# Optimization experiments

Measured on AMD Instinct MI355X. Metric: run time of the kernel, lower is better.

Reference implementation:

```python
import jax, jax.numpy as jnp
import numpy as np

EPS = 1e-5

def _layernorm(x, g, b):
    # LayerNorm over last dim (head_dim), eps=1e-5 like nn.LayerNorm
    mu = jnp.mean(x, axis=-1, keepdims=True)
    var = jnp.mean(jnp.square(x - mu), axis=-1, keepdims=True)
    return (x - mu) * jax.lax.rsqrt(var + EPS) * g + b

def _rotate_half(x):
    d = x.shape[-1] // 2
    return jnp.concatenate([-x[..., d:], x[..., :d]], axis=-1)

def _apply_rotary(x, cos, sin):
    # x: [B,S,H,D]; cos/sin: [S,D] broadcast over batch and heads
    c = cos[None, :, None, :]
    s = sin[None, :, None, :]
    return x * c + _rotate_half(x) * s

def setup_inputs() -> dict:
    key = jax.random.key(0)
    ks = jax.random.split(key, 16)
    B, S, Dm = 2, 1024, 2048
    H, Hkv, Dh = 16, 4, 128
    f = lambda k, shp: (jax.random.normal(k, shp, dtype=jnp.float32) * 0.02)
    return {
        "hidden_states": jax.random.normal(ks[0], (B, S, Dm), dtype=jnp.float32),
        "cos": jax.random.uniform(ks[1], (S, Dh), dtype=jnp.float32),
        "sin": jax.random.uniform(ks[2], (S, Dh), dtype=jnp.float32),
        "Wq": f(ks[3], (H * Dh, Dm)),   "bq": jnp.zeros((H * Dh,), jnp.float32),
        "Wk": f(ks[4], (Hkv * Dh, Dm)), "bk": jnp.zeros((Hkv * Dh,), jnp.float32),
        "Wv": f(ks[5], (Hkv * Dh, Dm)), "bv": jnp.zeros((Hkv * Dh,), jnp.float32),
        "Wo": f(ks[6], (Dm, H * Dh)),   "bo": jnp.zeros((Dm,), jnp.float32),
        "qn_g": jnp.ones((Dh,), jnp.float32), "qn_b": jnp.zeros((Dh,), jnp.float32),
        "kn_g": jnp.ones((Dh,), jnp.float32), "kn_b": jnp.zeros((Dh,), jnp.float32),
        "cu_seqlens": jnp.array([0, S, 2 * S], dtype=jnp.int32),
        "max_s": 1024,
    }

def reference(hidden_states, cos, sin, Wq, bq, Wk, bk, Wv, bv, Wo, bo,
              qn_g, qn_b, kn_g, kn_b, cu_seqlens, max_s):
    B, S, Dm = hidden_states.shape
    Dh = qn_g.shape[0]
    H = Wq.shape[0] // Dh
    Hkv = Wk.shape[0] // Dh
    scale = 1.0 / jnp.sqrt(jnp.float32(Dh))

    q = (hidden_states @ Wq.T + bq).reshape(B, S, H, Dh)
    k = (hidden_states @ Wk.T + bk).reshape(B, S, Hkv, Dh)
    v = (hidden_states @ Wv.T + bv).reshape(B, S, Hkv, Dh)

    q = _apply_rotary(_layernorm(q, qn_g, qn_b), cos, sin)
    k = _apply_rotary(_layernorm(k, kn_g, kn_b), cos, sin)

    # GQA: repeat_interleave kv heads to match q heads
    n_rep = H // Hkv
    if n_rep > 1:
        k = jnp.repeat(k, n_rep, axis=2)
        v = jnp.repeat(v, n_rep, axis=2)

    # scores: [B,H,S,S]
    scores = jnp.einsum('bqhd,bkhd->bhqk', q, k) * scale
    causal = jnp.tril(jnp.ones((S, S), dtype=bool))
    scores = jnp.where(causal[None, None], scores, jnp.finfo(scores.dtype).min)
    weights = jax.nn.softmax(scores, axis=-1)
    out = jnp.einsum('bhqk,bkhd->bqhd', weights, v).reshape(B, S, H * Dh)
    return out @ Wo.T + bo
```

## Files before the change

kernel.cpp:

```cpp
#include <hip/hip_runtime.h>
#include <cmath>

typedef __attribute__((ext_vector_type(8))) short bf16x8;
typedef __attribute__((ext_vector_type(4))) short s16x4;
typedef __attribute__((ext_vector_type(4))) float f32x4;

#define MFMA_BF16 __builtin_amdgcn_mfma_f32_16x16x32_bf16

__device__ __forceinline__ float bf2f(short s) {
    unsigned u = ((unsigned)(unsigned short)s) << 16;
    return __builtin_bit_cast(float, u);
}
__device__ __forceinline__ short f2bf(float f) {
    unsigned u = __builtin_bit_cast(unsigned, f);
    u += 0x7fffu + ((u >> 16) & 1u);
    return (short)(u >> 16);
}

__device__ __forceinline__ void gl_lds16(const short* gp, short* lp) {
    __builtin_amdgcn_global_load_lds(
        (const __attribute__((address_space(1))) unsigned int*)gp,
        (__attribute__((address_space(3))) unsigned int*)lp, 16, 0, 0);
}

__global__ __launch_bounds__(256) void cvt5(
    const float* s0, short* d0, int n0,
    const float* s1, short* d1, int n1,
    const float* s2, short* d2, int n2,
    const float* s3, short* d3, int n3,
    const float* s4, short* d4, int n4)
{
    long long i = (long long)blockIdx.x * 1024 + threadIdx.x * 4;
    const float* s; short* d;
    if      (i < n0)                  { s = s0; d = d0; }
    else if ((i -= n0) < n1)          { s = s1; d = d1; }
    else if ((i -= n1) < n2)          { s = s2; d = d2; }
    else if ((i -= n2) < n3)          { s = s3; d = d3; }
    else      { i -= n3;                s = s4; d = d4; }
    float4 v = *(const float4*)(s + i);
    s16x4 o;
    o[0] = f2bf(v.x); o[1] = f2bf(v.y); o[2] = f2bf(v.z); o[3] = f2bf(v.w);
    *(s16x4*)(d + i) = o;
}

__device__ __forceinline__ void stage128x32(
    const short* __restrict__ g, int gstride, short* l,
    int w, int lane, int kofs)
{
    const int row0 = 32 * w + (lane >> 2);
    const int kq   = (lane & 3) * 8;
#pragma unroll
    for (int i = 0; i < 2; i++) {
        const short* gp = g + (size_t)(row0 + 16 * i) * gstride + kofs + kq;
        short* lp = l + (32 * w + 16 * i) * 32 + lane * 8;
        gl_lds16(gp, lp);
    }
}

template <int MODE>
__global__ __launch_bounds__(256) void gemm128(
    const short* __restrict__ A, const short* __restrict__ W,
    const float* __restrict__ bq, const float* __restrict__ bk,
    const float* __restrict__ bv,
    short* __restrict__ qo, short* __restrict__ ko, short* __restrict__ vo,
    float* __restrict__ fo,
    int M, int K, int S, int Hkv, int Nq, int Nkv, int N)
{
    __shared__ __align__(16) short As[2][128 * 32];
    __shared__ __align__(16) short Bs[2][128 * 32];

    const int w    = threadIdx.x >> 6;
    const int lane = threadIdx.x & 63;
    const int l15  = lane & 15;
    const int quad = lane >> 4;
    const int wy   = w >> 1;
    const int wx   = w & 1;
    const int m0   = blockIdx.y * 128;
    const int n0   = blockIdx.x * 128;

    f32x4 acc[4][4];
#pragma unroll
    for (int i = 0; i < 4; i++)
#pragma unroll
        for (int j = 0; j < 4; j++) acc[i][j] = f32x4{0.f, 0.f, 0.f, 0.f};

    const short* Ab = A + (size_t)m0 * K;
    const short* Wb = W + (size_t)n0 * K;

    const int nk = K / 32;
    stage128x32(Ab, K, As[0], w, lane, 0);
    stage128x32(Wb, K, Bs[0], w, lane, 0);
    __syncthreads();

    for (int kt = 0; kt < nk; kt++) {
        const int cur = kt & 1;
        if (kt + 1 < nk) {
            stage128x32(Ab, K, As[cur ^ 1], w, lane, (kt + 1) * 32);
            stage128x32(Wb, K, Bs[cur ^ 1], w, lane, (kt + 1) * 32);
        }
        bf16x8 af[4], bfr[4];
#pragma unroll
        for (int i = 0; i < 4; i++)
            af[i] = *(const bf16x8*)(As[cur] + (wy * 64 + i * 16 + l15) * 32 + quad * 8);
#pragma unroll
        for (int j = 0; j < 4; j++)
            bfr[j] = *(const bf16x8*)(Bs[cur] + (wx * 64 + j * 16 + l15) * 32 + quad * 8);
#pragma unroll
        for (int i = 0; i < 4; i++)
#pragma unroll
            for (int j = 0; j < 4; j++)
                acc[i][j] = MFMA_BF16(af[i], bfr[j], acc[i][j], 0, 0, 0);
        __syncthreads();
    }

#pragma unroll
    for (int i = 0; i < 4; i++) {
#pragma unroll
        for (int j = 0; j < 4; j++) {
            const int col = n0 + wx * 64 + j * 16 + l15;
#pragma unroll
            for (int r = 0; r < 4; r++) {
                const int row = m0 + wy * 64 + i * 16 + quad * 4 + r;
                float v = acc[i][j][r];
                if constexpr (MODE == 0) {
                    if (col < Nq) {
                        qo[(size_t)row * Nq + col] = f2bf(v + bq[col]);
                    } else if (col < Nq + Nkv) {
                        int cn = col - Nq;
                        ko[(size_t)row * Nkv + cn] = f2bf(v + bk[cn]);
                    } else {
                        int cn = col - Nq - Nkv;
                        int b  = row / S, s = row - b * S;
                        int hk = cn >> 7, dh = cn & 127;
                        vo[(size_t)((b * Hkv + hk) * 128 + dh) * S + s] = f2bf(v + bv[cn]);
                    }
                } else {
                    fo[(size_t)row * N + col] = v + bq[col];
                }
            }
        }
    }
}

__global__ __launch_bounds__(256) void ln_rope(
    const short* __restrict__ X, short* __restrict__ Y,
    const float* __restrict__ g, const float* __restrict__ bta,
    const float* __restrict__ cosp, const float* __restrict__ sinp,
    int H, int S)
{
    const int gw   = blockIdx.x * 4 + (threadIdx.x >> 6);
    const int lane = threadIdx.x & 63;
    const int h  = gw % H;
    const int rs = gw / H;
    const int b  = rs / S;
    const int s  = rs - b * S;

    const short* x = X + ((size_t)rs * H + h) * 128;
    float x0 = bf2f(x[lane]), x1 = bf2f(x[lane + 64]);

    float sum = x0 + x1;
    float sq  = x0 * x0 + x1 * x1;
#pragma unroll
    for (int off = 32; off > 0; off >>= 1) {
        sum += __shfl_xor(sum, off, 64);
        sq  += __shfl_xor(sq, off, 64);
    }
    float mu  = sum * (1.f / 128.f);
    float var = sq * (1.f / 128.f) - mu * mu;
    float rinv = rsqrtf(var + 1e-5f);

    float y0 = (x0 - mu) * rinv * g[lane]      + bta[lane];
    float y1 = (x1 - mu) * rinv * g[lane + 64] + bta[lane + 64];

    float c0 = cosp[(size_t)s * 128 + lane];
    float c1 = cosp[(size_t)s * 128 + lane + 64];
    float s0 = sinp[(size_t)s * 128 + lane];
    float s1 = sinp[(size_t)s * 128 + lane + 64];

    float o0 = y0 * c0 - y1 * s0;
    float o1 = y1 * c1 + y0 * s1;

    short* yp = Y + ((size_t)(b * H + h) * S + s) * 128;
    yp[lane]      = f2bf(o0);
    yp[lane + 64] = f2bf(o1);
}

__global__ __launch_bounds__(256, 2) void attn(
    const short* __restrict__ Q, const short* __restrict__ Kt,
    const short* __restrict__ Vt, short* __restrict__ O,
    int S, int H, int Hkv, int nrep, float scale)
{
    __shared__ __align__(16) short Ks[2][16 * 512];
    __shared__ __align__(16) short Vs[2][16 * 512];
    __shared__ __align__(16) short P[4][16][72];

    const int w    = threadIdx.x >> 6;
    const int lane = threadIdx.x & 63;
    const int l15  = lane & 15;
    const int quad = lane >> 4;
    const int bh   = blockIdx.x;
    const int h    = bh % H;
    const int b    = bh / H;
    const int nyt  = gridDim.y;
    const int y    = blockIdx.y;
    const int qblk = (y < (nyt >> 1)) ? (nyt - 1 - y) : (y - (nyt >> 1));
    const int hk   = h / nrep;
    const int m0   = qblk * 64 + w * 16;
    const int qpos = m0 + l15;

    const short* qb = Q  + (size_t)(b * H + h) * S * 128;
    const short* kb = Kt + (size_t)(b * Hkv + hk) * S * 128;
    const short* vb = Vt + (size_t)(b * Hkv + hk) * 128 * S;

    auto stage = [&](int buf, int j0) {
#pragma unroll
        for (int i = 0; i < 8; i++) {
            if (w < 2) {
                const int s = w * 8 + i;
                const int t = s >> 2, c = s & 3;
                gl_lds16(kb + (size_t)(j0 + t * 16 + l15) * 128 + c * 32 + quad * 8,
                         Ks[buf] + s * 512 + lane * 8);
            } else {
                const int u = (w - 2) * 8 + i;
                const int c = u >> 1, hf = u & 1;
                gl_lds16(vb + (size_t)(c * 16 + l15) * S + j0 + hf * 32 + quad * 8,
                         Vs[buf] + u * 512 + lane * 8);
            }
        }
    };

    bf16x8 qf[4];
#pragma unroll
    for (int c = 0; c < 4; c++)
        qf[c] = *(const bf16x8*)(qb + (size_t)(m0 + l15) * 128 + c * 32 + quad * 8);

    f32x4 of[8];
#pragma unroll
    for (int c = 0; c < 8; c++) of[c] = f32x4{0.f, 0.f, 0.f, 0.f};
    float m_s = -1e30f, l_s = 0.f;
    const float c2 = scale * 1.44269504f;

    const int nkt = qblk + 1;
    stage(0, 0);
    __syncthreads();

    for (int kt = 0; kt < nkt; kt++) {
        const int cur = kt & 1;
        if (kt + 1 < nkt) stage(cur ^ 1, (kt + 1) * 64);

        const short* Kb = Ks[cur];
        const short* Vb = Vs[cur];
        const int j0 = kt * 64;

        f32x4 sc[4];
#pragma unroll
        for (int t = 0; t < 4; t++) sc[t] = f32x4{0.f, 0.f, 0.f, 0.f};
#pragma unroll
        for (int c = 0; c < 4; c++)
#pragma unroll
            for (int t = 0; t < 4; t++) {
                bf16x8 kf = *(const bf16x8*)(Kb + (t * 4 + c) * 512 + lane * 8);
                sc[t] = MFMA_BF16(kf, qf[c], sc[t], 0, 0, 0);
            }

        float v[4][4];
        float mx = -1e30f;
#pragma unroll
        for (int t = 0; t < 4; t++)
#pragma unroll
            for (int r = 0; r < 4; r++) {
                float s_ = sc[t][r];
                if (j0 + t * 16 + quad * 4 + r > qpos) s_ = -1e30f;
                v[t][r] = s_;
                mx = fmaxf(mx, s_);
            }
        mx = fmaxf(mx, __shfl_xor(mx, 16, 64));
        mx = fmaxf(mx, __shfl_xor(mx, 32, 64));
        float mnew  = fmaxf(m_s, mx);
        float mc    = mnew * c2;
        float alpha = exp2f(m_s * c2 - mc);
        float sum = 0.f;
        float p[4][4];
#pragma unroll
        for (int t = 0; t < 4; t++)
#pragma unroll
            for (int r = 0; r < 4; r++) {
                p[t][r] = exp2f(__builtin_fmaf(v[t][r], c2, -mc));
                sum += p[t][r];
            }
        sum += __shfl_xor(sum, 16, 64);
        sum += __shfl_xor(sum, 32, 64);
        l_s = l_s * alpha + sum;
        m_s = mnew;

#pragma unroll
        for (int c = 0; c < 8; c++) {
            f32x4 t = of[c];
            t[0] *= alpha; t[1] *= alpha; t[2] *= alpha; t[3] *= alpha;
            of[c] = t;
        }

#pragma unroll
        for (int t = 0; t < 4; t++) {
            s16x4 pk;
#pragma unroll
            for (int r = 0; r < 4; r++) pk[r] = f2bf(p[t][r]);
            *(s16x4*)(&P[w][l15][t * 16 + quad * 4]) = pk;
        }
        bf16x8 pb0 = *(const bf16x8*)(&P[w][l15][quad * 8]);
        bf16x8 pb1 = *(const bf16x8*)(&P[w][l15][32 + quad * 8]);

#pragma unroll
        for (int c = 0; c < 8; c++) {
            bf16x8 vf0 = *(const bf16x8*)(Vb + (c * 2 + 0) * 512 + lane * 8);
            bf16x8 vf1 = *(const bf16x8*)(Vb + (c * 2 + 1) * 512 + lane * 8);
            of[c] = MFMA_BF16(vf0, pb0, of[c], 0, 0, 0);
            of[c] = MFMA_BF16(vf1, pb1, of[c], 0, 0, 0);
        }
        __syncthreads();
    }

    const int HDh = H * 128;
    const float rinv = 1.0f / l_s;
    short* orow = O + ((size_t)b * S + qpos) * HDh + h * 128;
#pragma unroll
    for (int c = 0; c < 8; c++) {
        s16x4 ov;
#pragma unroll
        for (int r = 0; r < 4; r++) ov[r] = f2bf(of[c][r] * rinv);
        *(s16x4*)(orow + c * 16 + quad * 4) = ov;
    }
}

extern "C" void kernel_launch(void* const* d_in, const int* in_sizes, int n_in,
                              void* d_out, int out_size, void* d_ws, size_t ws_size,
                              hipStream_t stream) {
    const float* hs   = (const float*)d_in[0];
    const float* cosp = (const float*)d_in[1];
    const float* sinp = (const float*)d_in[2];
    const float* Wq   = (const float*)d_in[3];
    const float* bq   = (const float*)d_in[4];
    const float* Wk   = (const float*)d_in[5];
    const float* bk   = (const float*)d_in[6];
    const float* Wv   = (const float*)d_in[7];
    const float* bv   = (const float*)d_in[8];
    const float* Wo   = (const float*)d_in[9];
    const float* bo   = (const float*)d_in[10];
    const float* qg   = (const float*)d_in[11];
    const float* qb_  = (const float*)d_in[12];
    const float* kg   = (const float*)d_in[13];
    const float* kb_  = (const float*)d_in[14];

    const int Dh    = in_sizes[11];
    const int Dm    = in_sizes[10];
    const int HDh   = in_sizes[4];
    const int H     = HDh / Dh;
    const int HkvDh = in_sizes[6];
    const int Hkv   = HkvDh / Dh;
    const int S     = in_sizes[1] / Dh;
    const int B     = in_sizes[0] / (S * Dm);
    const int M     = B * S;
    const int nrep  = H / Hkv;

    char* ws = (char*)d_ws;
    short* hsb  = (short*)ws;  ws += (size_t)M * Dm      * 2;
    short* Wqb  = (short*)ws;  ws += (size_t)HDh * Dm    * 2;
    short* Wkb  = (short*)ws;  ws += (size_t)HkvDh * Dm  * 2;
    short* Wvb  = (short*)ws;  ws += (size_t)HkvDh * Dm  * 2;
    short* Wob  = (short*)ws;  ws += (size_t)Dm * HDh    * 2;
    short* qg16 = (short*)ws;  ws += (size_t)M * HDh     * 2;
    short* kg16 = (short*)ws;  ws += (size_t)M * HkvDh   * 2;
    short* qbuf = (short*)ws;  ws += (size_t)M * HDh     * 2;
    short* kbuf = (short*)ws;  ws += (size_t)M * HkvDh   * 2;
    short* vbuf = (short*)ws;  ws += (size_t)M * HkvDh   * 2;
    short* abuf = qg16;

    dim3 blk(256);
    const int n0 = M * Dm, n1 = HDh * Dm, n2 = HkvDh * Dm, n3 = HkvDh * Dm, n4 = Dm * HDh;
    cvt5<<<dim3((n0 + n1 + n2 + n3 + n4) / 1024), blk, 0, stream>>>(
        hs, hsb, n0, Wq, Wqb, n1, Wk, Wkb, n2, Wv, Wvb, n3, Wo, Wob, n4);

    const int Ntot = HDh + 2 * HkvDh;
    gemm128<0><<<dim3(Ntot / 128, M / 128), blk, 0, stream>>>(
        hsb, Wqb, bq, bk, bv, qg16, kg16, vbuf, nullptr,
        M, Dm, S, Hkv, HDh, HkvDh, Ntot);

    ln_rope<<<dim3(M * H / 4),   blk, 0, stream>>>(qg16, qbuf, qg, qb_, cosp, sinp, H,   S);
    ln_rope<<<dim3(M * Hkv / 4), blk, 0, stream>>>(kg16, kbuf, kg, kb_, cosp, sinp, Hkv, S);

    const float scale = 1.0f / sqrtf((float)Dh);
    attn<<<dim3(H * B, S / 64), blk, 0, stream>>>(qbuf, kbuf, vbuf, abuf, S, H, Hkv, nrep, scale);

    gemm128<1><<<dim3(Dm / 128, M / 128), blk, 0, stream>>>(
        abuf, Wob, bo, nullptr, nullptr, nullptr, nullptr, nullptr, (float*)d_out,
        M, HDh, S, Hkv, Dm, 0, Dm);
}
```

Baseline: 270.6 us.

## Shrink GEMM tile to 128x64 with XOR-swizzled LDS and fuse LN-rope launches

```diff
diff --git a/kernel.cpp b/kernel.cpp
--- a/kernel.cpp
+++ b/kernel.cpp
@@ -43,22 +43,8 @@
     *(s16x4*)(d + i) = o;
 }
 
-__device__ __forceinline__ void stage128x32(
-    const short* __restrict__ g, int gstride, short* l,
-    int w, int lane, int kofs)
-{
-    const int row0 = 32 * w + (lane >> 2);
-    const int kq   = (lane & 3) * 8;
-#pragma unroll
-    for (int i = 0; i < 2; i++) {
-        const short* gp = g + (size_t)(row0 + 16 * i) * gstride + kofs + kq;
-        short* lp = l + (32 * w + 16 * i) * 32 + lane * 8;
-        gl_lds16(gp, lp);
-    }
-}
-
 template <int MODE>
-__global__ __launch_bounds__(256) void gemm128(
+__global__ __launch_bounds__(256) void gemm_t(
     const short* __restrict__ A, const short* __restrict__ W,
     const float* __restrict__ bq, const float* __restrict__ bk,
     const float* __restrict__ bv,
@@ -66,8 +52,8 @@
     float* __restrict__ fo,
     int M, int K, int S, int Hkv, int Nq, int Nkv, int N)
 {
-    __shared__ __align__(16) short As[2][128 * 32];
-    __shared__ __align__(16) short Bs[2][128 * 32];
+    __shared__ __align__(16) short As[2][8 * 512];
+    __shared__ __align__(16) short Bs[2][4 * 512];
 
     const int w    = threadIdx.x >> 6;
     const int lane = threadIdx.x & 63;
@@ -76,39 +62,50 @@
     const int wy   = w >> 1;
     const int wx   = w & 1;
     const int m0   = blockIdx.y * 128;
-    const int n0   = blockIdx.x * 128;
-
-    f32x4 acc[4][4];
-#pragma unroll
-    for (int i = 0; i < 4; i++)
-#pragma unroll
-        for (int j = 0; j < 4; j++) acc[i][j] = f32x4{0.f, 0.f, 0.f, 0.f};
+    const int n0   = blockIdx.x * 64;
 
     const short* Ab = A + (size_t)m0 * K;
     const short* Wb = W + (size_t)n0 * K;
 
+    const int srow = lane >> 2;
+    const int scol = ((lane & 3) ^ (srow & 3)) * 8;
+    auto stage = [&](int buf, int kofs) {
+#pragma unroll
+        for (int i = 0; i < 2; i++) {
+            const int c = 2 * w + i;
+            gl_lds16(Ab + (size_t)(c * 16 + srow) * K + kofs + scol,
+                     As[buf] + c * 512 + lane * 8);
+        }
+        gl_lds16(Wb + (size_t)(w * 16 + srow) * K + kofs + scol,
+                 Bs[buf] + w * 512 + lane * 8);
+    };
+
+    f32x4 acc[4][2];
+#pragma unroll
+    for (int i = 0; i < 4; i++)
+#pragma unroll
+        for (int j = 0; j < 2; j++) acc[i][j] = f32x4{0.f, 0.f, 0.f, 0.f};
+
+    const int ridx = (l15 * 4 + (quad ^ (l15 & 3))) * 8;
     const int nk = K / 32;
-    stage128x32(Ab, K, As[0], w, lane, 0);
-    stage128x32(Wb, K, Bs[0], w, lane, 0);
+    stage(0, 0);
     __syncthreads();
 
     for (int kt = 0; kt < nk; kt++) {
         const int cur = kt & 1;
-        if (kt + 1 < nk) {
-            stage128x32(Ab, K, As[cur ^ 1], w, lane, (kt + 1) * 32);
-            stage128x32(Wb, K, Bs[cur ^ 1], w, lane, (kt + 1) * 32);
-        }
-        bf16x8 af[4], bfr[4];
+        if (kt + 1 < nk) stage(cur ^ 1, (kt + 1) * 32);
+
+        bf16x8 af[4], bfr[2];
 #pragma unroll
         for (int i = 0; i < 4; i++)
-            af[i] = *(const bf16x8*)(As[cur] + (wy * 64 + i * 16 + l15) * 32 + quad * 8);
-#pragma unroll
-        for (int j = 0; j < 4; j++)
-            bfr[j] = *(const bf16x8*)(Bs[cur] + (wx * 64 + j * 16 + l15) * 32 + quad * 8);
+            af[i] = *(const bf16x8*)(As[cur] + (wy * 4 + i) * 512 + ridx);
+#pragma unroll
+        for (int j = 0; j < 2; j++)
+            bfr[j] = *(const bf16x8*)(Bs[cur] + (wx * 2 + j) * 512 + ridx);
 #pragma unroll
         for (int i = 0; i < 4; i++)
 #pragma unroll
-            for (int j = 0; j < 4; j++)
+            for (int j = 0; j < 2; j++)
                 acc[i][j] = MFMA_BF16(af[i], bfr[j], acc[i][j], 0, 0, 0);
         __syncthreads();
     }
@@ -116,8 +113,8 @@
 #pragma unroll
     for (int i = 0; i < 4; i++) {
 #pragma unroll
-        for (int j = 0; j < 4; j++) {
-            const int col = n0 + wx * 64 + j * 16 + l15;
+        for (int j = 0; j < 2; j++) {
+            const int col = n0 + wx * 32 + j * 16 + l15;
 #pragma unroll
             for (int r = 0; r < 4; r++) {
                 const int row = m0 + wy * 64 + i * 16 + quad * 4 + r;
@@ -142,20 +139,26 @@
     }
 }
 
-__global__ __launch_bounds__(256) void ln_rope(
-    const short* __restrict__ X, short* __restrict__ Y,
-    const float* __restrict__ g, const float* __restrict__ bta,
+__global__ __launch_bounds__(256) void ln_rope2(
+    const short* __restrict__ Xq, short* __restrict__ Yq,
+    const short* __restrict__ Xk, short* __restrict__ Yk,
+    const float* __restrict__ qg, const float* __restrict__ qbe,
+    const float* __restrict__ kg, const float* __restrict__ kbe,
     const float* __restrict__ cosp, const float* __restrict__ sinp,
-    int H, int S)
+    int H, int Hkv, int S, int nq)
 {
-    const int gw   = blockIdx.x * 4 + (threadIdx.x >> 6);
+    int gw = blockIdx.x * 4 + (threadIdx.x >> 6);
     const int lane = threadIdx.x & 63;
-    const int h  = gw % H;
-    const int rs = gw / H;
+    const short* X; short* Y; const float* g; const float* bt; int Hc;
+    if (gw < nq) { X = Xq; Y = Yq; g = qg; bt = qbe; Hc = H; }
+    else { gw -= nq; X = Xk; Y = Yk; g = kg; bt = kbe; Hc = Hkv; }
+
+    const int h  = gw % Hc;
+    const int rs = gw / Hc;
     const int b  = rs / S;
     const int s  = rs - b * S;
 
-    const short* x = X + ((size_t)rs * H + h) * 128;
+    const short* x = X + ((size_t)rs * Hc + h) * 128;
     float x0 = bf2f(x[lane]), x1 = bf2f(x[lane + 64]);
 
     float sum = x0 + x1;
@@ -169,8 +172,8 @@
     float var = sq * (1.f / 128.f) - mu * mu;
     float rinv = rsqrtf(var + 1e-5f);
 
-    float y0 = (x0 - mu) * rinv * g[lane]      + bta[lane];
-    float y1 = (x1 - mu) * rinv * g[lane + 64] + bta[lane + 64];
+    float y0 = (x0 - mu) * rinv * g[lane]      + bt[lane];
+    float y1 = (x1 - mu) * rinv * g[lane + 64] + bt[lane + 64];
 
     float c0 = cosp[(size_t)s * 128 + lane];
     float c1 = cosp[(size_t)s * 128 + lane + 64];
@@ -180,7 +183,7 @@
     float o0 = y0 * c0 - y1 * s0;
     float o1 = y1 * c1 + y0 * s1;
 
-    short* yp = Y + ((size_t)(b * H + h) * S + s) * 128;
+    short* yp = Y + ((size_t)(b * Hc + h) * S + s) * 128;
     yp[lane]      = f2bf(o0);
     yp[lane + 64] = f2bf(o1);
 }
@@ -381,17 +384,18 @@
         hs, hsb, n0, Wq, Wqb, n1, Wk, Wkb, n2, Wv, Wvb, n3, Wo, Wob, n4);
 
     const int Ntot = HDh + 2 * HkvDh;
-    gemm128<0><<<dim3(Ntot / 128, M / 128), blk, 0, stream>>>(
+    gemm_t<0><<<dim3(Ntot / 64, M / 128), blk, 0, stream>>>(
         hsb, Wqb, bq, bk, bv, qg16, kg16, vbuf, nullptr,
         M, Dm, S, Hkv, HDh, HkvDh, Ntot);
 
-    ln_rope<<<dim3(M * H / 4),   blk, 0, stream>>>(qg16, qbuf, qg, qb_, cosp, sinp, H,   S);
-    ln_rope<<<dim3(M * Hkv / 4), blk, 0, stream>>>(kg16, kbuf, kg, kb_, cosp, sinp, Hkv, S);
+    const int nq = M * H;
+    ln_rope2<<<dim3((nq + M * Hkv) / 4), blk, 0, stream>>>(
+        qg16, qbuf, kg16, kbuf, qg, qb_, kg, kb_, cosp, sinp, H, Hkv, S, nq);
 
     const float scale = 1.0f / sqrtf((float)Dh);
     attn<<<dim3(H * B, S / 64), blk, 0, stream>>>(qbuf, kbuf, vbuf, abuf, S, H, Hkv, nrep, scale);
 
-    gemm128<1><<<dim3(Dm / 128, M / 128), blk, 0, stream>>>(
+    gemm_t<1><<<dim3(Dm / 64, M / 128), blk, 0, stream>>>(
         abuf, Wob, bo, nullptr, nullptr, nullptr, nullptr, nullptr, (float*)d_out,
         M, HDh, S, Hkv, Dm, 0, Dm);
 }
```

Measured after the change: 256.2 us. 1.06x faster.
